# Kernel optimization log

Hardware: AMD Instinct MI355X
Metric: run time of the kernel (lower is better)

The kernel has to match this reference:

```python
import jax, jax.numpy as jnp
import numpy as np

N_OBJ = 100000
E = 64
SMOOTH = 12.0  # MAXIMUM_SMOOTHNESS


def _mish(x):
    return x * jnp.tanh(jax.nn.softplus(x))


def _mlp(x, wi, bi, wo, bo):
    # torch.nn.Linear convention: y = x @ W.T + b
    return jnp.dot(_mish(jnp.dot(x, wi.T) + bi), wo.T) + bo


def _linear_init(key, out_dim, in_dim):
    s = 1.0 / np.sqrt(in_dim)
    kw, kb = jax.random.split(key)
    w = jax.random.uniform(kw, (out_dim, in_dim), jnp.float32, -s, s)
    b = jax.random.uniform(kb, (out_dim,), jnp.float32, -s, s)
    return w, b


def setup_inputs() -> dict:
    key = jax.random.key(0)
    ks = jax.random.split(key, 16)
    inp = {}
    inp["object_embeddings"] = jax.random.normal(ks[0], (N_OBJ, E), jnp.float32)
    inp["idx_unary"] = jax.random.randint(ks[1], (200000,), 0, N_OBJ, jnp.int32)
    inp["idx_binary"] = jax.random.randint(ks[2], (600000,), 0, N_OBJ, jnp.int32)
    inp["idx_ternary"] = jax.random.randint(ks[3], (300000,), 0, N_OBJ, jnp.int32)
    k = 4
    for name, ar in [("unary", 1), ("binary", 2), ("ternary", 3)]:
        d = ar * E
        wi, bi = _linear_init(ks[k], d, d)
        wo, bo = _linear_init(ks[k + 1], d, d)
        inp[f"{name}_wi"], inp[f"{name}_bi"] = wi, bi
        inp[f"{name}_wo"], inp[f"{name}_bo"] = wo, bo
        k += 2
    # update MLP: Linear(2E,2E) then Linear(2E,E)
    inp["upd_wi"], inp["upd_bi"] = _linear_init(ks[k], 2 * E, 2 * E)
    inp["upd_wo"], inp["upd_bo"] = _linear_init(ks[k + 1], E, 2 * E)
    return inp


def reference(object_embeddings, idx_unary, idx_binary, idx_ternary,
              unary_wi, unary_bi, unary_wo, unary_bo,
              binary_wi, binary_bi, binary_wo, binary_bo,
              ternary_wi, ternary_bi, ternary_wo, ternary_bo,
              upd_wi, upd_bi, upd_wo, upd_bo):
    def rel_msg(idx, arity, wi, bi, wo, bo):
        x = object_embeddings[idx].reshape(-1, arity * E)  # gather
        m = x + _mlp(x, wi, bi, wo, bo)                    # residual per-relation MLP
        return m.reshape(-1, E)

    msgs = jnp.concatenate([
        rel_msg(idx_unary, 1, unary_wi, unary_bi, unary_wo, unary_bo),
        rel_msg(idx_binary, 2, binary_wi, binary_bi, binary_wo, binary_bo),
        rel_msg(idx_ternary, 3, ternary_wi, ternary_bi, ternary_wo, ternary_bo),
    ], axis=0)
    inds = jnp.concatenate([idx_unary, idx_binary, idx_ternary], axis=0)

    # scatter-amax (include_self=False -> untouched rows stay 0, like torch zeros init)
    mx = jax.ops.segment_max(msgs, inds, num_segments=N_OBJ)
    mx = jnp.where(jnp.isneginf(mx), 0.0, mx)
    mx = jax.lax.stop_gradient(mx)

    exps = jnp.exp(SMOOTH * (msgs - mx[inds]))
    s = jax.ops.segment_sum(exps, inds, num_segments=N_OBJ) + 1e-16
    max_msg = jnp.log(s) / SMOOTH + mx  # smooth log-sum-exp aggregation

    upd_in = jnp.concatenate([max_msg, object_embeddings], axis=1)
    return object_embeddings + _mlp(upd_in, upd_wi, upd_bi, upd_wo, upd_bo)
```

## Files before the change

### kernel.cpp

```cpp
#include <hip/hip_runtime.h>
#include <math.h>

#define NOBJ 100000
#define SMOOTH 12.0f

typedef __attribute__((ext_vector_type(8))) short bf16x8;
typedef __attribute__((ext_vector_type(4))) float f32x4;
typedef unsigned short u16;
typedef unsigned int u32;
typedef unsigned long long u64;

#define OFF_UWI 0
#define OFF_UWO 4096
#define OFF_BWI 8192
#define OFF_BWO 24576
#define OFF_TWI 40960
#define OFF_TWO 77824
#define OFF_PWI 114688
#define OFF_PWO 131072
#define WTOT    139264
__device__ u16 g_wbf[WTOT];

__device__ __forceinline__ u16 f2b(float x) {
    union { float f; u32 u; } v; v.f = x;
    u32 r = v.u + 0x7FFFu + ((v.u >> 16) & 1);
    return (u16)(r >> 16);
}
__device__ __forceinline__ float b2f(u16 b) {
    union { u32 u; float f; } v; v.u = ((u32)b) << 16; return v.f;
}
__device__ __forceinline__ float mish_fast(float x) {
    float e = __expf(fminf(x, 15.f));
    float t = __builtin_fmaf(e, e, 2.f * e);
    return x * t * __builtin_amdgcn_rcpf(t + 2.f);
}
__device__ __forceinline__ double exp12_f64(float m) {
    float t = m * (SMOOTH * 1.4426950408889634f);
    float n = floorf(t);
    float f = exp2f(t - n);
    return ldexp((double)f, (int)n);
}
__device__ __forceinline__ float lse_from_sum(double S) {
    if (S == 0.0) return -3.0701134573253942f;
    union { double d; u64 u; } vu; vu.d = S;
    int k = (int)((vu.u >> 52) & 0x7FF) - 1022;
    vu.u = (vu.u & 0x000FFFFFFFFFFFFFULL) | 0x3FE0000000000000ULL;
    float fr = (float)vu.d;
    return ((float)k + __log2f(fr)) * 0.057762265046662105f;
}

__global__ void prep_kernel(const float* __restrict__ uwi, const float* __restrict__ uwo,
                            const float* __restrict__ bwi, const float* __restrict__ bwo,
                            const float* __restrict__ twi, const float* __restrict__ two_,
                            const float* __restrict__ pwi, const float* __restrict__ pwo,
                            const float* __restrict__ emb, u16* __restrict__ emb_bf,
                            u32* __restrict__ counts, u32* __restrict__ cursor) {
    int i = blockIdx.x * 256 + threadIdx.x;
    if (i < WTOT) {
        const float* src; int off;
        if      (i < OFF_UWO) { src = uwi; off = OFF_UWI; }
        else if (i < OFF_BWI) { src = uwo; off = OFF_UWO; }
        else if (i < OFF_BWO) { src = bwi; off = OFF_BWI; }
        else if (i < OFF_TWI) { src = bwo; off = OFF_BWO; }
        else if (i < OFF_TWO) { src = twi; off = OFF_TWI; }
        else if (i < OFF_PWI) { src = two_; off = OFF_TWO; }
        else if (i < OFF_PWO) { src = pwi; off = OFF_PWI; }
        else                  { src = pwo; off = OFF_PWO; }
        g_wbf[i] = f2b(src[i - off]);
    }
    if (i < NOBJ * 16) {
        float4 v = ((const float4*)emb)[i];
        ushort4 o;
        o.x = f2b(v.x); o.y = f2b(v.y); o.z = f2b(v.z); o.w = f2b(v.w);
        ((ushort4*)emb_bf)[i] = o;
    }
    if (counts && i < NOBJ) { counts[i] = 0u; cursor[i] = 0u; }
}

__device__ __forceinline__ int lookup_obj(long long m,
                                          const int* __restrict__ iu, int nU,
                                          const int* __restrict__ ib, int nB,
                                          const int* __restrict__ it) {
    if (m < nU) return iu[m];
    m -= nU;
    if (m < nB) return ib[m];
    return it[m - nB];
}

__global__ void hist_kernel(const int* __restrict__ iu, int nU,
                            const int* __restrict__ ib, int nB,
                            const int* __restrict__ it, int nT,
                            u32* __restrict__ counts) {
    long long t = (long long)blockIdx.x * 256 + threadIdx.x;
    if (t >= (long long)nU + nB + nT) return;
    atomicAdd(&counts[lookup_obj(t, iu, nU, ib, nB, it)], 1u);
}

__global__ void scan1_kernel(const u32* __restrict__ counts, u32* __restrict__ offs,
                             u32* __restrict__ bsum) {
    __shared__ u32 s[256];
    int t = threadIdx.x;
    int g = blockIdx.x * 256 + t;
    u32 v = (g < NOBJ) ? counts[g] : 0u;
    s[t] = v; __syncthreads();
    for (int off = 1; off < 256; off <<= 1) {
        u32 x = (t >= off) ? s[t - off] : 0u; __syncthreads();
        s[t] += x; __syncthreads();
    }
    if (g < NOBJ) offs[g] = s[t] - v;
    if (t == 255) bsum[blockIdx.x] = s[255];
}

__global__ void scan2_kernel(u32* __restrict__ bsum, int nblk) {
    __shared__ u32 s[512];
    int t = threadIdx.x;
    u32 v = (t < nblk) ? bsum[t] : 0u;
    s[t] = v; __syncthreads();
    for (int off = 1; off < 512; off <<= 1) {
        u32 x = (t >= off) ? s[t - off] : 0u; __syncthreads();
        s[t] += x; __syncthreads();
    }
    if (t < nblk) bsum[t] = s[t] - v;
}

__global__ void slot_kernel(const int* __restrict__ iu, int nU,
                            const int* __restrict__ ib, int nB,
                            const int* __restrict__ it, int nT,
                            const u32* __restrict__ offs, const u32* __restrict__ bsum,
                            u32* __restrict__ cursor, u32* __restrict__ slotByRef) {
    long long t = (long long)blockIdx.x * 256 + threadIdx.x;
    if (t >= (long long)nU + nB + nT) return;
    int obj = lookup_obj(t, iu, nU, ib, nB, it);
    u32 pos = atomicAdd(&cursor[obj], 1u);
    slotByRef[t] = offs[obj] + bsum[obj >> 8] + pos;
}

template<int D, int MW, int MODE, int WOFF_I, int WOFF_O>
__global__ __launch_bounds__(64 * MW)
void rel_pass_mfma(const u16* __restrict__ emb_bf,
                   const int* __restrict__ idx, int nRows,
                   const float* __restrict__ bi, const float* __restrict__ bo,
                   double* __restrict__ ssum64,
                   u16* __restrict__ msgs_out, const u32* __restrict__ slotByRef,
                   long long baseRef) {
    constexpr int ARITY = D / 64;
    constexpr int NT = D / 16;
    constexpr int NSC = D / 64;
    constexpr int M = MW * 16;
    __shared__ u16 xs[M * D];
    __shared__ u16 wlds[D * 64];
    __shared__ int objsm[M * ARITY];
    __shared__ u32 slotm[M * ARITY];

    const int tid = threadIdx.x;
    const int w = tid >> 6, l = tid & 63;
    const int lo = l & 15, hi = l >> 4;
    const int row0 = blockIdx.x * M;

    for (int i = tid; i < M * ARITY; i += 64 * MW) {
        int row = row0 + i / ARITY;
        bool ok = (row < nRows);
        objsm[i] = ok ? idx[(size_t)row * ARITY + i % ARITY] : -1;
        if (MODE == 3)
            slotm[i] = ok ? slotByRef[baseRef + (long long)row0 * ARITY + i] : 0xFFFFFFFFu;
    }
    __syncthreads();

    for (int i = tid; i < M * D / 8; i += 64 * MW) {
        int r = i / (D / 8), c8 = i % (D / 8);
        int obj = objsm[r * ARITY + (c8 >> 3)];
        bf16x8 v = {0, 0, 0, 0, 0, 0, 0, 0};
        if (obj >= 0) v = *(const bf16x8*)(emb_bf + (size_t)obj * 64 + (c8 & 7) * 8);
        *(bf16x8*)&xs[(r * D + c8 * 8) ^ ((r & 7) << 3)] = v;
    }

    f32x4 acc[NT];
    const int arow = w * 16 + lo;
    const int asw = (arow & 7) << 3;

#pragma unroll
    for (int n = 0; n < NT; ++n) { float b = bi[n * 16 + lo]; acc[n] = (f32x4){b, b, b, b}; }
#pragma unroll
    for (int sc = 0; sc < NSC; ++sc) {
        __syncthreads();
        for (int i = tid; i < D * 8; i += 64 * MW) {
            int u = i * 8;
            int j = u >> 6;
            bf16x8 v = *(const bf16x8*)&g_wbf[WOFF_I + j * D + sc * 64 + (u & 63)];
            *(bf16x8*)&wlds[u ^ ((j & 7) << 3)] = v;
        }
        __syncthreads();
#pragma unroll
        for (int kkL = 0; kkL < 2; ++kkL) {
            bf16x8 a = *(const bf16x8*)&xs[(arow * D + (sc * 2 + kkL) * 32 + hi * 8) ^ asw];
#pragma unroll
            for (int n = 0; n < NT; ++n) {
                int j = n * 16 + lo;
                bf16x8 b = *(const bf16x8*)&wlds[(j * 64 + kkL * 32 + hi * 8) ^ ((j & 7) << 3)];
                acc[n] = __builtin_amdgcn_mfma_f32_16x16x32_bf16(a, b, acc[n], 0, 0, 0);
            }
        }
    }

#pragma unroll
    for (int n = 0; n < NT; ++n) {
        float bov = bo[n * 16 + lo];
#pragma unroll
        for (int r = 0; r < 4; ++r) {
            int row = w * 16 + hi * 4 + r;
            int col = n * 16 + lo;
            int sidx = (row * D + col) ^ ((row & 7) << 3);
            float xv = b2f(xs[sidx]);
            xs[sidx] = f2b(mish_fast(acc[n][r]));
            acc[n][r] = bov + xv;
        }
    }

#pragma unroll
    for (int sc = 0; sc < NSC; ++sc) {
        __syncthreads();
        for (int i = tid; i < D * 8; i += 64 * MW) {
            int u = i * 8;
            int j = u >> 6;
            bf16x8 v = *(const bf16x8*)&g_wbf[WOFF_O + j * D + sc * 64 + (u & 63)];
            *(bf16x8*)&wlds[u ^ ((j & 7) << 3)] = v;
        }
        __syncthreads();
#pragma unroll
        for (int kkL = 0; kkL < 2; ++kkL) {
            bf16x8 a = *(const bf16x8*)&xs[(arow * D + (sc * 2 + kkL) * 32 + hi * 8) ^ asw];
#pragma unroll
            for (int n = 0; n < NT; ++n) {
                int j = n * 16 + lo;
                bf16x8 b = *(const bf16x8*)&wlds[(j * 64 + kkL * 32 + hi * 8) ^ ((j & 7) << 3)];
                acc[n] = __builtin_amdgcn_mfma_f32_16x16x32_bf16(a, b, acc[n], 0, 0, 0);
            }
        }
    }

    if (MODE == 3) {
#pragma unroll
        for (int n = 0; n < NT; ++n) {
            int col = n * 16 + lo;
#pragma unroll
            for (int r = 0; r < 4; ++r) {
                int row = w * 16 + hi * 4 + r;
                _Float16 hv = (_Float16)acc[n][r];
                xs[(row * D + col) ^ ((row & 7) << 3)] = *(u16*)&hv;
            }
        }
        __syncthreads();
        for (int i = tid; i < M * D / 8; i += 64 * MW) {
            int u = i * 8;
            int row = u / D, off = u - row * D;
            u32 slot = slotm[row * ARITY + (off >> 6)];
            if (slot == 0xFFFFFFFFu) continue;
            *(bf16x8*)(msgs_out + (size_t)slot * 64 + (off & 63)) =
                *(const bf16x8*)&xs[u ^ ((row & 7) << 3)];
        }
    } else {
#pragma unroll
        for (int n = 0; n < NT; ++n) {
            int col = n * 16 + lo;
#pragma unroll
            for (int r = 0; r < 4; ++r) {
                int row = w * 16 + hi * 4 + r;
                int obj = objsm[row * ARITY + (col >> 6)];
                if (obj < 0) continue;
                unsafeAtomicAdd(&ssum64[(size_t)obj * 64 + (col & 63)], exp12_f64(acc[n][r]));
            }
        }
    }
}

__global__ __launch_bounds__(256)
void agg_update(const float* __restrict__ emb, const u16* __restrict__ msgs,
                const u32* __restrict__ offs, const u32* __restrict__ bsum,
                const u32* __restrict__ counts,
                const float* __restrict__ bi, const float* __restrict__ bo,
                float* __restrict__ out) {
    __shared__ u16 uin[64 * 128];
    __shared__ u16 h[64 * 128];
    const int tid = threadIdx.x;
    const int w = tid >> 6, l = tid & 63, lo = l & 15, hi = l >> 4;
    const int row0 = blockIdx.x * 64;

    for (int rr = 0; rr < 16; ++rr) {
        int row = w * 16 + rr;
        int obj = row0 + row;
        float lse = -3.0701134573253942f, ev = 0.f;
        if (obj < NOBJ) {
            u32 off = offs[obj] + bsum[obj >> 8], n = counts[obj];
            const u16* mrow = msgs + (size_t)off * 64 + l;
            double S0 = 0.0, S1 = 0.0;
            u32 j = 0;
            for (; j + 4 <= n; j += 4) {
                float v0 = (float)(*(const _Float16*)(mrow + (size_t)(j + 0) * 64));
                float v1 = (float)(*(const _Float16*)(mrow + (size_t)(j + 1) * 64));
                float v2 = (float)(*(const _Float16*)(mrow + (size_t)(j + 2) * 64));
                float v3 = (float)(*(const _Float16*)(mrow + (size_t)(j + 3) * 64));
                S0 += exp12_f64(v0); S1 += exp12_f64(v1);
                S0 += exp12_f64(v2); S1 += exp12_f64(v3);
            }
            for (; j < n; ++j)
                S0 += exp12_f64((float)(*(const _Float16*)(mrow + (size_t)j * 64)));
            lse = lse_from_sum(S0 + S1);
            ev = emb[(size_t)obj * 64 + l];
        }
        uin[(row * 128 + l) ^ ((row & 7) << 3)] = f2b(lse);
        uin[(row * 128 + 64 + l) ^ ((row & 7) << 3)] = f2b(ev);
    }
    __syncthreads();

    const int arow = w * 16 + lo;
    const int asw = (arow & 7) << 3;
    f32x4 acc[8];
#pragma unroll
    for (int n = 0; n < 8; ++n) { float b = bi[n * 16 + lo]; acc[n] = (f32x4){b, b, b, b}; }
#pragma unroll
    for (int kk = 0; kk < 4; ++kk) {
        bf16x8 a = *(const bf16x8*)&uin[(arow * 128 + kk * 32 + hi * 8) ^ asw];
#pragma unroll
        for (int n = 0; n < 8; ++n) {
            bf16x8 b = *(const bf16x8*)&g_wbf[OFF_PWI + (n * 16 + lo) * 128 + kk * 32 + hi * 8];
            acc[n] = __builtin_amdgcn_mfma_f32_16x16x32_bf16(a, b, acc[n], 0, 0, 0);
        }
    }
#pragma unroll
    for (int n = 0; n < 8; ++n) {
#pragma unroll
        for (int r = 0; r < 4; ++r) {
            int row = w * 16 + hi * 4 + r;
            int col = n * 16 + lo;
            h[(row * 128 + col) ^ ((row & 7) << 3)] = f2b(mish_fast(acc[n][r]));
        }
    }
    __syncthreads();

    f32x4 acc2[4];
#pragma unroll
    for (int n = 0; n < 4; ++n) { float b = bo[n * 16 + lo]; acc2[n] = (f32x4){b, b, b, b}; }
#pragma unroll
    for (int kk = 0; kk < 4; ++kk) {
        bf16x8 a = *(const bf16x8*)&h[(arow * 128 + kk * 32 + hi * 8) ^ asw];
#pragma unroll
        for (int n = 0; n < 4; ++n) {
            bf16x8 b = *(const bf16x8*)&g_wbf[OFF_PWO + (n * 16 + lo) * 128 + kk * 32 + hi * 8];
            acc2[n] = __builtin_amdgcn_mfma_f32_16x16x32_bf16(a, b, acc2[n], 0, 0, 0);
        }
    }
#pragma unroll
    for (int n = 0; n < 4; ++n) {
        int col = n * 16 + lo;
#pragma unroll
        for (int r = 0; r < 4; ++r) {
            int row = w * 16 + hi * 4 + r;
            int obj = row0 + row;
            if (obj < NOBJ)
                out[(size_t)obj * 64 + col] = emb[(size_t)obj * 64 + col] + acc2[n][r];
        }
    }
}

__global__ __launch_bounds__(256)
void update_mfma_f64(const float* __restrict__ emb, const double* __restrict__ ssum64,
                     const float* __restrict__ bi, const float* __restrict__ bo,
                     float* __restrict__ out) {
    __shared__ u16 uin[64 * 128];
    __shared__ u16 h[64 * 128];
    const int tid = threadIdx.x;
    const int w = tid >> 6, l = tid & 63, lo = l & 15, hi = l >> 4;
    const int row0 = blockIdx.x * 64;

    for (int i = tid; i < 64 * 128; i += 256) {
        int r = i >> 7, c = i & 127;
        int obj = row0 + r;
        float v = 0.f;
        if (obj < NOBJ) {
            if (c < 64) v = lse_from_sum(ssum64[(size_t)obj * 64 + c]);
            else v = emb[(size_t)obj * 64 + (c - 64)];
        }
        uin[i ^ ((r & 7) << 3)] = f2b(v);
    }
    __syncthreads();

    const int arow = w * 16 + lo;
    const int asw = (arow & 7) << 3;
    f32x4 acc[8];
#pragma unroll
    for (int n = 0; n < 8; ++n) { float b = bi[n * 16 + lo]; acc[n] = (f32x4){b, b, b, b}; }
#pragma unroll
    for (int kk = 0; kk < 4; ++kk) {
        bf16x8 a = *(const bf16x8*)&uin[(arow * 128 + kk * 32 + hi * 8) ^ asw];
#pragma unroll
        for (int n = 0; n < 8; ++n) {
            bf16x8 b = *(const bf16x8*)&g_wbf[OFF_PWI + (n * 16 + lo) * 128 + kk * 32 + hi * 8];
            acc[n] = __builtin_amdgcn_mfma_f32_16x16x32_bf16(a, b, acc[n], 0, 0, 0);
        }
    }
#pragma unroll
    for (int n = 0; n < 8; ++n) {
#pragma unroll
        for (int r = 0; r < 4; ++r) {
            int row = w * 16 + hi * 4 + r;
            int col = n * 16 + lo;
            h[(row * 128 + col) ^ ((row & 7) << 3)] = f2b(mish_fast(acc[n][r]));
        }
    }
    __syncthreads();
    f32x4 acc2[4];
#pragma unroll
    for (int n = 0; n < 4; ++n) { float b = bo[n * 16 + lo]; acc2[n] = (f32x4){b, b, b, b}; }
#pragma unroll
    for (int kk = 0; kk < 4; ++kk) {
        bf16x8 a = *(const bf16x8*)&h[(arow * 128 + kk * 32 + hi * 8) ^ asw];
#pragma unroll
        for (int n = 0; n < 4; ++n) {
            bf16x8 b = *(const bf16x8*)&g_wbf[OFF_PWO + (n * 16 + lo) * 128 + kk * 32 + hi * 8];
            acc2[n] = __builtin_amdgcn_mfma_f32_16x16x32_bf16(a, b, acc2[n], 0, 0, 0);
        }
    }
#pragma unroll
    for (int n = 0; n < 4; ++n) {
        int col = n * 16 + lo;
#pragma unroll
        for (int r = 0; r < 4; ++r) {
            int row = w * 16 + hi * 4 + r;
            int obj = row0 + row;
            if (obj < NOBJ)
                out[(size_t)obj * 64 + col] = emb[(size_t)obj * 64 + col] + acc2[n][r];
        }
    }
}

static inline size_t align256(size_t x) { return (x + 255) & ~(size_t)255; }

extern "C" void kernel_launch(void* const* d_in, const int* in_sizes, int n_in,
                              void* d_out, int out_size, void* d_ws, size_t ws_size,
                              hipStream_t stream) {
    const float* emb = (const float*)d_in[0];
    const int* iu = (const int*)d_in[1];
    const int* ib = (const int*)d_in[2];
    const int* it = (const int*)d_in[3];
    const float* uwi = (const float*)d_in[4];
    const float* ubi = (const float*)d_in[5];
    const float* uwo = (const float*)d_in[6];
    const float* ubo = (const float*)d_in[7];
    const float* bwi = (const float*)d_in[8];
    const float* bbi = (const float*)d_in[9];
    const float* bwo = (const float*)d_in[10];
    const float* bbo = (const float*)d_in[11];
    const float* twi = (const float*)d_in[12];
    const float* tbi = (const float*)d_in[13];
    const float* two_ = (const float*)d_in[14];
    const float* tbo = (const float*)d_in[15];
    const float* pwi = (const float*)d_in[16];
    const float* pbi = (const float*)d_in[17];
    const float* pwo = (const float*)d_in[18];
    const float* pbo = (const float*)d_in[19];

    const int nU = in_sizes[1];
    const int nB = in_sizes[2];
    const int nT = in_sizes[3];
    const int rowsU = nU;
    const int rowsB = nB / 2;
    const int rowsT = nT / 3;
    const long long NREF = (long long)nU + nB + nT;

    const size_t seg = (size_t)NOBJ * 64;
    const int gU = (rowsU + 63) / 64;
    const int gB = (rowsB + 63) / 64;
    const int gT = (rowsT + 63) / 64;
    const int nblkScan = (NOBJ + 255) / 256;
    const int gPrep = (NOBJ * 16 + 255) / 256;

    char* p = (char*)d_ws;
    u16* msgs = (u16*)p;        p += align256(2 * (size_t)NREF * 64);
    u32* counts = (u32*)p;      p += align256(4 * (size_t)NOBJ);
    u32* offs = (u32*)p;        p += align256(4 * (size_t)NOBJ);
    u32* cursor = (u32*)p;      p += align256(4 * (size_t)NOBJ);
    u32* bsum = (u32*)p;        p += align256(4 * 512);
    u32* slotByRef = (u32*)p;   p += align256(4 * (size_t)NREF);
    u16* emb_bf = (u16*)p;      p += align256(2 * seg);
    const size_t need = (size_t)(p - (char*)d_ws);

    if (ws_size >= need) {
        prep_kernel<<<gPrep, 256, 0, stream>>>(uwi, uwo, bwi, bwo, twi, two_, pwi, pwo,
                                               emb, emb_bf, counts, cursor);
        int gRef = (int)((NREF + 255) / 256);
        hist_kernel<<<gRef, 256, 0, stream>>>(iu, nU, ib, nB, it, nT, counts);
        scan1_kernel<<<nblkScan, 256, 0, stream>>>(counts, offs, bsum);
        scan2_kernel<<<1, 512, 0, stream>>>(bsum, nblkScan);
        slot_kernel<<<gRef, 256, 0, stream>>>(iu, nU, ib, nB, it, nT, offs, bsum, cursor, slotByRef);

        rel_pass_mfma<64, 4, 3, OFF_UWI, OFF_UWO><<<gU, 256, 0, stream>>>(
            emb_bf, iu, rowsU, ubi, ubo, nullptr, msgs, slotByRef, 0LL);
        rel_pass_mfma<128, 4, 3, OFF_BWI, OFF_BWO><<<gB, 256, 0, stream>>>(
            emb_bf, ib, rowsB, bbi, bbo, nullptr, msgs, slotByRef, (long long)nU);
        rel_pass_mfma<192, 4, 3, OFF_TWI, OFF_TWO><<<gT, 256, 0, stream>>>(
            emb_bf, it, rowsT, tbi, tbo, nullptr, msgs, slotByRef, (long long)(nU + nB));

        agg_update<<<(NOBJ + 63) / 64, 256, 0, stream>>>(
            emb, msgs, offs, bsum, counts, pbi, pbo, (float*)d_out);
    } else {
        double* ssum64 = (double*)d_ws;
        u16* emb_bf2 = (u16*)((char*)d_ws + seg * sizeof(double));
        prep_kernel<<<gPrep, 256, 0, stream>>>(uwi, uwo, bwi, bwo, twi, two_, pwi, pwo,
                                               emb, emb_bf2, nullptr, nullptr);
        hipMemsetAsync(ssum64, 0, seg * sizeof(double), stream);
        rel_pass_mfma<64, 4, 2, OFF_UWI, OFF_UWO><<<gU, 256, 0, stream>>>(
            emb_bf2, iu, rowsU, ubi, ubo, ssum64, nullptr, nullptr, 0);
        rel_pass_mfma<128, 4, 2, OFF_BWI, OFF_BWO><<<gB, 256, 0, stream>>>(
            emb_bf2, ib, rowsB, bbi, bbo, ssum64, nullptr, nullptr, 0);
        rel_pass_mfma<192, 4, 2, OFF_TWI, OFF_TWO><<<gT, 256, 0, stream>>>(
            emb_bf2, it, rowsT, tbi, tbo, ssum64, nullptr, nullptr, 0);
        update_mfma_f64<<<(NOBJ + 63) / 64, 256, 0, stream>>>(
            emb, ssum64, pbi, pbo, (float*)d_out);
    }
}
```

Measured before the change: 387.2 us.

## Vectorize per-object message reduction with 16-byte loads and butterfly shuffle sums

In agg_update, each row's message sum now loads 8 half values per lane with one 16-byte load, so the 64 lanes cover 8 message rows per step instead of one 2-byte load per lane per message. The eight per-lane partial sums are combined across lanes with an xor-shuffle transpose and routed back through a small per-wave shared buffer. Offsets and counts are preloaded once per wave and broadcast with shuffles, removing per-row scalar loads. Because each wave now only touches its own 16 rows, the block-wide barriers are dropped and the hidden-layer buffer reuses the input tile, which cuts shared memory. This relies on wave-local ordering of shared memory accesses, which is correct only if no lane reads another wave's rows.

```diff
diff --git a/kernel.cpp b/kernel.cpp
--- a/kernel.cpp
+++ b/kernel.cpp
@@ -280,37 +280,64 @@
                 const float* __restrict__ bi, const float* __restrict__ bo,
                 float* __restrict__ out) {
     __shared__ u16 uin[64 * 128];
-    __shared__ u16 h[64 * 128];
+    __shared__ double colsum[4][64];
     const int tid = threadIdx.x;
     const int w = tid >> 6, l = tid & 63, lo = l & 15, hi = l >> 4;
+    const int rl = l >> 3, c8 = l & 7;
     const int row0 = blockIdx.x * 64;
+
+    u32 off_l = 0, n_l = 0;
+    {
+        int o = row0 + w * 16 + lo;
+        if (hi == 0 && o < NOBJ) { off_l = offs[o] + bsum[o >> 8]; n_l = counts[o]; }
+    }
 
     for (int rr = 0; rr < 16; ++rr) {
         int row = w * 16 + rr;
         int obj = row0 + row;
         float lse = -3.0701134573253942f, ev = 0.f;
         if (obj < NOBJ) {
-            u32 off = offs[obj] + bsum[obj >> 8], n = counts[obj];
-            const u16* mrow = msgs + (size_t)off * 64 + l;
-            double S0 = 0.0, S1 = 0.0;
-            u32 j = 0;
-            for (; j + 4 <= n; j += 4) {
-                float v0 = (float)(*(const _Float16*)(mrow + (size_t)(j + 0) * 64));
-                float v1 = (float)(*(const _Float16*)(mrow + (size_t)(j + 1) * 64));
-                float v2 = (float)(*(const _Float16*)(mrow + (size_t)(j + 2) * 64));
-                float v3 = (float)(*(const _Float16*)(mrow + (size_t)(j + 3) * 64));
-                S0 += exp12_f64(v0); S1 += exp12_f64(v1);
-                S0 += exp12_f64(v2); S1 += exp12_f64(v3);
+            u32 off = __shfl(off_l, rr);
+            u32 n = __shfl(n_l, rr);
+            double s[8] = {0.0, 0.0, 0.0, 0.0, 0.0, 0.0, 0.0, 0.0};
+            for (u32 j = 0; j < n; j += 8) {
+                if (j + (u32)rl < n) {
+                    bf16x8 v = *(const bf16x8*)(msgs + (size_t)(off + j + rl) * 64 + c8 * 8);
+#pragma unroll
+                    for (int k = 0; k < 8; ++k) {
+                        u16 hb = (u16)v[k];
+                        float f = (float)(*(const _Float16*)&hb);
+                        s[k] += exp12_f64(f);
+                    }
+                }
             }
-            for (; j < n; ++j)
-                S0 += exp12_f64((float)(*(const _Float16*)(mrow + (size_t)j * 64)));
-            lse = lse_from_sum(S0 + S1);
+            double t0 = __shfl_xor(s[0], 8), t1 = __shfl_xor(s[1], 8);
+            double t2 = __shfl_xor(s[2], 8), t3 = __shfl_xor(s[3], 8);
+            double t4 = __shfl_xor(s[4], 8), t5 = __shfl_xor(s[5], 8);
+            double t6 = __shfl_xor(s[6], 8), t7 = __shfl_xor(s[7], 8);
+            bool bb0 = (rl & 1) != 0;
+            double a0 = bb0 ? (s[4] + t4) : (s[0] + t0);
+            double a1 = bb0 ? (s[5] + t5) : (s[1] + t1);
+            double a2 = bb0 ? (s[6] + t6) : (s[2] + t2);
+            double a3 = bb0 ? (s[7] + t7) : (s[3] + t3);
+            double u0 = __shfl_xor(a0, 16), u1 = __shfl_xor(a1, 16);
+            double u2 = __shfl_xor(a2, 16), u3 = __shfl_xor(a3, 16);
+            bool bb1 = (rl & 2) != 0;
+            double c0 = bb1 ? (a2 + u2) : (a0 + u0);
+            double c1 = bb1 ? (a3 + u3) : (a1 + u1);
+            double v0 = __shfl_xor(c0, 32), v1 = __shfl_xor(c1, 32);
+            double dfin = ((rl & 4) != 0) ? (c1 + v1) : (c0 + v0);
+            int col = c8 * 8 + ((rl & 1) << 2) + (rl & 2) + ((rl >> 2) & 1);
+            colsum[w][col] = dfin;
+            asm volatile("s_waitcnt lgkmcnt(0)" ::: "memory");
+            __builtin_amdgcn_sched_barrier(0);
+            double S = colsum[w][l];
+            lse = lse_from_sum(S);
             ev = emb[(size_t)obj * 64 + l];
         }
         uin[(row * 128 + l) ^ ((row & 7) << 3)] = f2b(lse);
         uin[(row * 128 + 64 + l) ^ ((row & 7) << 3)] = f2b(ev);
     }
-    __syncthreads();
 
     const int arow = w * 16 + lo;
     const int asw = (arow & 7) << 3;
@@ -332,17 +359,16 @@
         for (int r = 0; r < 4; ++r) {
             int row = w * 16 + hi * 4 + r;
             int col = n * 16 + lo;
-            h[(row * 128 + col) ^ ((row & 7) << 3)] = f2b(mish_fast(acc[n][r]));
-        }
-    }
-    __syncthreads();
+            uin[(row * 128 + col) ^ ((row & 7) << 3)] = f2b(mish_fast(acc[n][r]));
+        }
+    }
 
     f32x4 acc2[4];
 #pragma unroll
     for (int n = 0; n < 4; ++n) { float b = bo[n * 16 + lo]; acc2[n] = (f32x4){b, b, b, b}; }
 #pragma unroll
     for (int kk = 0; kk < 4; ++kk) {
-        bf16x8 a = *(const bf16x8*)&h[(arow * 128 + kk * 32 + hi * 8) ^ asw];
+        bf16x8 a = *(const bf16x8*)&uin[(arow * 128 + kk * 32 + hi * 8) ^ asw];
 #pragma unroll
         for (int n = 0; n < 4; ++n) {
             bf16x8 b = *(const bf16x8*)&g_wbf[OFF_PWO + (n * 16 + lo) * 128 + kk * 32 + hi * 8];
```

Result: no change. 389.5 us (+0.6%).

## Split aggregation into a per-object kernel, then run the update MLP

Applied to the files above, without the earlier changes.

The fused agg_update kernel, which looped serially over 16 objects per wave, is split in two. agg_kernel gives each object its own wave, spread across many more blocks, and uses four independent f64 accumulators. It writes the log-sum-exp rows into the output buffer, and a separate update_from_lse kernel reads them back for the MLP. The aim is more parallelism and latency hiding in the gather-and-exp reduction, at the cost of an extra kernel launch and a 25.6MB fp32 round trip through global memory. update_from_lse reads lsein from the same buffer it writes out, which looks safe because each block reads its own rows before the barrier.

```diff
diff --git a/kernel.cpp b/kernel.cpp
--- a/kernel.cpp
+++ b/kernel.cpp
@@ -274,41 +274,54 @@
 }
 
 __global__ __launch_bounds__(256)
-void agg_update(const float* __restrict__ emb, const u16* __restrict__ msgs,
+void agg_kernel(const u16* __restrict__ msgs,
                 const u32* __restrict__ offs, const u32* __restrict__ bsum,
                 const u32* __restrict__ counts,
-                const float* __restrict__ bi, const float* __restrict__ bo,
-                float* __restrict__ out) {
+                float* __restrict__ lse_out) {
+    int o = blockIdx.x * 4 + (threadIdx.x >> 6);
+    int l = threadIdx.x & 63;
+    if (o >= NOBJ) return;
+    u32 off = offs[o] + bsum[o >> 8];
+    u32 n = counts[o];
+    const u16* mrow = msgs + (size_t)off * 64 + l;
+    double S0 = 0.0, S1 = 0.0, S2 = 0.0, S3 = 0.0;
+    u32 j = 0;
+    for (; j + 4 <= n; j += 4) {
+        u16 h0 = mrow[(size_t)(j + 0) * 64];
+        u16 h1 = mrow[(size_t)(j + 1) * 64];
+        u16 h2 = mrow[(size_t)(j + 2) * 64];
+        u16 h3 = mrow[(size_t)(j + 3) * 64];
+        S0 += exp12_f64((float)(*(const _Float16*)&h0));
+        S1 += exp12_f64((float)(*(const _Float16*)&h1));
+        S2 += exp12_f64((float)(*(const _Float16*)&h2));
+        S3 += exp12_f64((float)(*(const _Float16*)&h3));
+    }
+    for (; j < n; ++j) {
+        u16 h = mrow[(size_t)j * 64];
+        S0 += exp12_f64((float)(*(const _Float16*)&h));
+    }
+    lse_out[(size_t)o * 64 + l] = lse_from_sum((S0 + S1) + (S2 + S3));
+}
+
+__global__ __launch_bounds__(256)
+void update_from_lse(const float* __restrict__ emb, const float* lsein,
+                     const float* __restrict__ bi, const float* __restrict__ bo,
+                     float* out) {
     __shared__ u16 uin[64 * 128];
     __shared__ u16 h[64 * 128];
     const int tid = threadIdx.x;
     const int w = tid >> 6, l = tid & 63, lo = l & 15, hi = l >> 4;
     const int row0 = blockIdx.x * 64;
 
-    for (int rr = 0; rr < 16; ++rr) {
-        int row = w * 16 + rr;
-        int obj = row0 + row;
-        float lse = -3.0701134573253942f, ev = 0.f;
+    for (int i = tid; i < 64 * 128; i += 256) {
+        int r = i >> 7, c = i & 127;
+        int obj = row0 + r;
+        float v = 0.f;
         if (obj < NOBJ) {
-            u32 off = offs[obj] + bsum[obj >> 8], n = counts[obj];
-            const u16* mrow = msgs + (size_t)off * 64 + l;
-            double S0 = 0.0, S1 = 0.0;
-            u32 j = 0;
-            for (; j + 4 <= n; j += 4) {
-                float v0 = (float)(*(const _Float16*)(mrow + (size_t)(j + 0) * 64));
-                float v1 = (float)(*(const _Float16*)(mrow + (size_t)(j + 1) * 64));
-                float v2 = (float)(*(const _Float16*)(mrow + (size_t)(j + 2) * 64));
-                float v3 = (float)(*(const _Float16*)(mrow + (size_t)(j + 3) * 64));
-                S0 += exp12_f64(v0); S1 += exp12_f64(v1);
-                S0 += exp12_f64(v2); S1 += exp12_f64(v3);
-            }
-            for (; j < n; ++j)
-                S0 += exp12_f64((float)(*(const _Float16*)(mrow + (size_t)j * 64)));
-            lse = lse_from_sum(S0 + S1);
-            ev = emb[(size_t)obj * 64 + l];
-        }
-        uin[(row * 128 + l) ^ ((row & 7) << 3)] = f2b(lse);
-        uin[(row * 128 + 64 + l) ^ ((row & 7) << 3)] = f2b(ev);
+            if (c < 64) v = lsein[(size_t)obj * 64 + c];
+            else v = emb[(size_t)obj * 64 + (c - 64)];
+        }
+        uin[i ^ ((r & 7) << 3)] = f2b(v);
     }
     __syncthreads();
 
@@ -336,7 +349,6 @@
         }
     }
     __syncthreads();
-
     f32x4 acc2[4];
 #pragma unroll
     for (int n = 0; n < 4; ++n) { float b = bo[n * 16 + lo]; acc2[n] = (f32x4){b, b, b, b}; }
@@ -500,8 +512,10 @@
         rel_pass_mfma<192, 4, 3, OFF_TWI, OFF_TWO><<<gT, 256, 0, stream>>>(
             emb_bf, it, rowsT, tbi, tbo, nullptr, msgs, slotByRef, (long long)(nU + nB));
 
-        agg_update<<<(NOBJ + 63) / 64, 256, 0, stream>>>(
-            emb, msgs, offs, bsum, counts, pbi, pbo, (float*)d_out);
+        float* lsebuf = (float*)d_out;
+        agg_kernel<<<(NOBJ + 3) / 4, 256, 0, stream>>>(msgs, offs, bsum, counts, lsebuf);
+        update_from_lse<<<(NOBJ + 63) / 64, 256, 0, stream>>>(
+            emb, lsebuf, pbi, pbo, (float*)d_out);
     } else {
         double* ssum64 = (double*)d_ws;
         u16* emb_bf2 = (u16*)((char*)d_ws + seg * sizeof(double));
```

After: 374.0 us. -3.4%, faster.
